# Kernel tuning notes

Measured on AMD Instinct MI355X. Metric: run time of the kernel, lower is better.

Reference implementation:

```python
import jax, jax.numpy as jnp
import numpy as np

D_MODEL = 1024
SEQ_LEN = 4096


def setup_inputs() -> dict:
    key = jax.random.key(0)
    ks = jax.random.split(key, 7)
    s = 1.0 / np.sqrt(D_MODEL)
    return {
        "x": jax.random.normal(ks[0], (SEQ_LEN, D_MODEL), dtype=jnp.float32),
        "w_q": jax.random.normal(ks[1], (D_MODEL, D_MODEL), dtype=jnp.float32) * s,
        "b_q": jax.random.normal(ks[2], (D_MODEL,), dtype=jnp.float32) * s,
        "w_k": jax.random.normal(ks[3], (D_MODEL, D_MODEL), dtype=jnp.float32) * s,
        "b_k": jax.random.normal(ks[4], (D_MODEL,), dtype=jnp.float32) * s,
        "w_v": jax.random.normal(ks[5], (D_MODEL, D_MODEL), dtype=jnp.float32) * s,
        "b_v": jax.random.normal(ks[6], (D_MODEL,), dtype=jnp.float32) * s,
    }


def reference(x, w_q, b_q, w_k, b_k, w_v, b_v):
    # q/k/v: [S, D]; torch Linear computes x @ W.T + b, weights here stored as [D, D]
    q = x @ w_q.T + b_q
    k = x @ w_k.T + b_k
    v = x @ w_v.T + b_v
    temperature = jnp.asarray(D_MODEL, dtype=x.dtype) ** 0.5
    # scores: [S, S]
    attn = jax.nn.softmax((q / temperature) @ k.T, axis=-1)
    # dropout is identity in eval mode
    return attn @ v
```

## Files before the change

kernel.cpp:

```cpp
#include <hip/hip_runtime.h>
#include <hip/hip_bf16.h>
#include <stdint.h>

#define SEQ 4096
#define DM  1024

typedef __attribute__((ext_vector_type(8))) short  s16x8;
typedef __attribute__((ext_vector_type(8))) _Float16 h16x8;
typedef __attribute__((ext_vector_type(4))) float  f32x4;

__device__ __forceinline__ ushort f2bf(float f) {
    union { float f; uint32_t u; } x; x.f = f;
    uint32_t r = x.u + 0x7fffu + ((x.u >> 16) & 1u);
    return (ushort)(r >> 16);
}

__device__ __forceinline__ void gload16(const void* g, void* l) {
    __builtin_amdgcn_global_load_lds(
        (const __attribute__((address_space(1))) void*)g,
        (__attribute__((address_space(3))) void*)l,
        16, 0, 0);
}

__global__ __launch_bounds__(256) void cvt_bf16(const float* __restrict__ in,
                                                ushort* __restrict__ out, int n4) {
    int i = blockIdx.x * blockDim.x + threadIdx.x;
    if (i < n4) {
        float4 v = ((const float4*)in)[i];
        ushort4 o;
        o.x = f2bf(v.x); o.y = f2bf(v.y); o.z = f2bf(v.z); o.w = f2bf(v.w);
        ((ushort4*)out)[i] = o;
    }
}

__global__ __launch_bounds__(512, 1)
void gemm256_score(const ushort* __restrict__ Q, const ushort* __restrict__ Km,
                   _Float16* __restrict__ S)
{
    constexpr int NT = DM / 64;
    constexpr int TOTAL_H = NT * 4;
    __shared__ ushort lds_u[65536];
    char* lb = (char*)lds_u;

    const int wg = blockIdx.x;
    const int logical = (wg & 7) * 32 + (wg >> 3);
    const int bx = logical & 15;
    const int by = logical >> 4;
    const int m0 = by * 256, n0 = bx * 256;

    const int tid = threadIdx.x;
    const int w = tid >> 6, l = tid & 63;
    const int wr = w >> 2, wc = w & 3;
    const int lm = l & 15;
    const int khb = (l >> 4) * 16;

    const ushort* Ab = Q  + (size_t)m0 * DM;
    const ushort* Bb = Km + (size_t)n0 * DM;

    const int in0 = tid * 16, in1 = 8192 + tid * 16;
    const int b0 = in0 ^ (((in0 >> 9) & 1) << 5);
    const int b1 = in1 ^ (((in1 >> 9) & 1) << 5);
    const int r0_ = b0 >> 6, c0_ = (b0 & 63) >> 1;
    const int r1_ = b1 >> 6, c1_ = (b1 & 63) >> 1;

    const int swzb = ((lm >> 3) & 1) << 5;
    const int aoff = (((wr * 128 + lm) * 64 + khb) ^ swzb);
    const int boff = (((wc * 64 + lm) * 64 + khb) ^ swzb);

    f32x4 acc[8][4] = {};
    s16x8 bq[4];

#define RBASE(buf, region) ((buf) * 65536 + (region) * 16384)

#define STAGE_H(g) do { \
    const int hidx_ = (g) - 1; const int tile_ = hidx_ >> 2; const int reg_ = hidx_ & 3; \
    const ushort* mp_ = (reg_ & 1) ? Bb : Ab; \
    const int colb_ = tile_ * 64 + (reg_ >> 1) * 32; \
    char* dst_ = lb + RBASE(tile_ & 1, reg_); \
    gload16(mp_ + (size_t)r0_ * DM + colb_ + c0_, dst_ + in0); \
    gload16(mp_ + (size_t)r1_ * DM + colb_ + c1_, dst_ + in1); \
} while (0)

#define PHASE(ph, kt2) do { \
    constexpr int kk_   = (((ph) - 1) >> 1) & 1; \
    constexpr int mh_   = ((ph) - 1) & 1; \
    constexpr int rbuf_ = ((ph) <= 4) ? 0 : 1; \
    constexpr int areg_ = kk_ * 2; \
    constexpr int breg_ = kk_ * 2 + 1; \
    s16x8 aq[4]; \
    if (mh_ == 0) { \
        _Pragma("unroll") \
        for (int nj = 0; nj < 4; ++nj) \
            bq[nj] = *(const s16x8*)(lb + RBASE(rbuf_, breg_) + boff + nj * 1024); \
    } \
    _Pragma("unroll") \
    for (int i = 0; i < 4; ++i) \
        aq[i] = *(const s16x8*)(lb + RBASE(rbuf_, areg_) + aoff + (mh_ * 4 + i) * 1024); \
    { const int g_ = (kt2) * 8 + (ph) + 6; if (g_ <= TOTAL_H) STAGE_H(g_); } \
    __builtin_amdgcn_s_barrier(); \
    asm volatile("s_waitcnt lgkmcnt(0)" ::: "memory"); \
    __builtin_amdgcn_sched_barrier(0); \
    __builtin_amdgcn_s_setprio(1); \
    _Pragma("unroll") \
    for (int i = 0; i < 4; ++i) { \
        _Pragma("unroll") \
        for (int nj = 0; nj < 4; ++nj) \
            acc[mh_ * 4 + i][nj] = __builtin_amdgcn_mfma_f32_16x16x32_bf16( \
                aq[i], bq[nj], acc[mh_ * 4 + i][nj], 0, 0, 0); \
    } \
    __builtin_amdgcn_s_setprio(0); \
    if ((ph) == 4 || (ph) == 8) asm volatile("s_waitcnt vmcnt(4)" ::: "memory"); \
    __builtin_amdgcn_s_barrier(); \
} while (0)

    STAGE_H(1); STAGE_H(2); STAGE_H(3); STAGE_H(4); STAGE_H(5); STAGE_H(6);
    asm volatile("s_waitcnt vmcnt(4)" ::: "memory");
    __builtin_amdgcn_s_barrier();

    for (int kt2 = 0; kt2 < NT / 2; ++kt2) {
        PHASE(1, kt2); PHASE(2, kt2); PHASE(3, kt2); PHASE(4, kt2);
        PHASE(5, kt2); PHASE(6, kt2); PHASE(7, kt2); PHASE(8, kt2);
    }

    const int er0 = m0 + wr * 128 + (l >> 4) * 4;
    const int ec0 = n0 + wc * 64 + lm;
#pragma unroll
    for (int mi = 0; mi < 8; ++mi)
#pragma unroll
        for (int nj = 0; nj < 4; ++nj)
#pragma unroll
            for (int r = 0; r < 4; ++r)
                S[(size_t)(er0 + mi * 16 + r) * SEQ + ec0 + nj * 16] =
                    (_Float16)acc[mi][nj][r];
#undef PHASE
#undef STAGE_H
#undef RBASE
}

template<int BIAS_MODE, int OUT_MODE>
__global__ __launch_bounds__(256)
void gemm128(const ushort* __restrict__ A, int lda,
             const ushort* __restrict__ B, int ldb,
             const float* __restrict__ bias,
             void* __restrict__ Cout, int ldc,
             int K, float scale, int nbx)
{
    __shared__ ushort lds_u[32768];
    char* lb = (char*)lds_u;

    const int nwg = gridDim.x;
    const int wg  = blockIdx.x;
    const int logical = (wg & 7) * (nwg >> 3) + (wg >> 3);
    const int bx = logical % nbx, by = logical / nbx;
    const int m0 = by * 128, n0 = bx * 128;

    const int tid = threadIdx.x;
    const int w = tid >> 6, l = tid & 63;
    const int wm = (w >> 1) * 64, wn = (w & 1) * 64;
    const int lm = l & 15;
    const int khb = (l >> 4) * 16;
    const int swzb = ((lm >> 3) & 1) << 5;
    const int aoff = ((wm + lm) * 64 + khb) ^ swzb;
    const int boff = ((wn + lm) * 64 + khb) ^ swzb;

    int rr[4], cc[4];
#pragma unroll
    for (int i = 0; i < 4; ++i) {
        const int rest = (i & 1) * 4096 + tid * 16;
        const int b = rest ^ (((rest >> 9) & 1) << 5);
        rr[i] = b >> 6; cc[i] = (b & 63) >> 1;
    }

#define STAGE128(t_, buf_) do { \
    const int colt_ = (t_) * 64; \
    _Pragma("unroll") \
    for (int i = 0; i < 4; ++i) { \
        const int ldso_ = (i >> 1) * 8192 + (i & 1) * 4096 + tid * 16; \
        gload16(A + (size_t)(m0 + rr[i]) * lda + colt_ + (i >> 1) * 32 + cc[i], \
                lb + (buf_) * 32768 + ldso_); \
        gload16(B + (size_t)(n0 + rr[i]) * ldb + colt_ + (i >> 1) * 32 + cc[i], \
                lb + (buf_) * 32768 + 16384 + ldso_); \
    } \
} while (0)

    f32x4 acc[4][4] = {};

#define COMPUTE128(buf_) do { \
    _Pragma("unroll") \
    for (int kk = 0; kk < 2; ++kk) { \
        s16x8 a_[4], b_[4]; \
        _Pragma("unroll") \
        for (int i = 0; i < 4; ++i) \
            a_[i] = *(const s16x8*)(lb + (buf_) * 32768 + kk * 8192 + aoff + i * 1024); \
        _Pragma("unroll") \
        for (int j = 0; j < 4; ++j) \
            b_[j] = *(const s16x8*)(lb + (buf_) * 32768 + 16384 + kk * 8192 + boff + j * 1024); \
        _Pragma("unroll") \
        for (int i = 0; i < 4; ++i) { \
            _Pragma("unroll") \
            for (int j = 0; j < 4; ++j) \
                acc[i][j] = __builtin_amdgcn_mfma_f32_16x16x32_bf16(a_[i], b_[j], acc[i][j], 0, 0, 0); \
        } \
    } \
} while (0)

    const int NT = K / 64;
    STAGE128(0, 0);
    __syncthreads();
    int t = 0;
    for (; t + 2 < NT; t += 2) {
        STAGE128(t + 1, 1); COMPUTE128(0); __syncthreads();
        STAGE128(t + 2, 0); COMPUTE128(1); __syncthreads();
    }
    STAGE128(NT - 1, 1); COMPUTE128(0); __syncthreads();
    COMPUTE128(1);

    const int r0 = m0 + wm + ((l >> 4) << 2);
    const int c0 = n0 + wn + lm;
#pragma unroll
    for (int i = 0; i < 4; ++i) {
#pragma unroll
        for (int j = 0; j < 4; ++j) {
#pragma unroll
            for (int r = 0; r < 4; ++r) {
                const int row = r0 + i * 16 + r;
                const int col = c0 + j * 16;
                float v = acc[i][j][r];
                if (BIAS_MODE == 1) v += bias[col];
                if (BIAS_MODE == 2) v += bias[row];
                v *= scale;
                if (OUT_MODE == 0) ((float*)Cout)[(size_t)row * ldc + col] = v;
                else               ((ushort*)Cout)[(size_t)row * ldc + col] = f2bf(v);
            }
        }
    }
#undef STAGE128
#undef COMPUTE128
}

__global__ __launch_bounds__(256) void softmax_rows(void* __restrict__ Sbase) {
    const int row = blockIdx.x;
    const int tid = threadIdx.x;
    const _Float16* srow = (const _Float16*)Sbase + (size_t)row * SEQ;

    float f[16];
#pragma unroll
    for (int j = 0; j < 2; ++j) {
        h16x8 v = *(const h16x8*)(srow + (size_t)(tid + j * 256) * 8);
#pragma unroll
        for (int e = 0; e < 8; ++e) f[j * 8 + e] = (float)v[e];
    }

    float m = f[0];
#pragma unroll
    for (int i = 1; i < 16; ++i) m = fmaxf(m, f[i]);
#pragma unroll
    for (int off = 32; off > 0; off >>= 1) m = fmaxf(m, __shfl_xor(m, off));

    __shared__ float redm[4], reds[4];
    const int w = tid >> 6, l = tid & 63;
    if (l == 0) redm[w] = m;
    __syncthreads();
    m = fmaxf(fmaxf(redm[0], redm[1]), fmaxf(redm[2], redm[3]));

    float s = 0.f;
#pragma unroll
    for (int i = 0; i < 16; ++i) { f[i] = __expf(f[i] - m); s += f[i]; }
#pragma unroll
    for (int off = 32; off > 0; off >>= 1) s += __shfl_xor(s, off);
    if (l == 0) reds[w] = s;
    __syncthreads();
    s = (reds[0] + reds[1]) + (reds[2] + reds[3]);
    const float inv = 1.0f / s;

    ushort* prow = (ushort*)Sbase + (size_t)row * SEQ;
#pragma unroll
    for (int j = 0; j < 2; ++j) {
        s16x8 o;
#pragma unroll
        for (int e = 0; e < 8; ++e) o[e] = (short)f2bf(f[j * 8 + e] * inv);
        *(s16x8*)(prow + (size_t)(tid + j * 256) * 8) = o;
    }
}

extern "C" void kernel_launch(void* const* d_in, const int* in_sizes, int n_in,
                              void* d_out, int out_size, void* d_ws, size_t ws_size,
                              hipStream_t stream)
{
    const float* x  = (const float*)d_in[0];
    const float* wq = (const float*)d_in[1];
    const float* bq = (const float*)d_in[2];
    const float* wk = (const float*)d_in[3];
    const float* bk = (const float*)d_in[4];
    const float* wv = (const float*)d_in[5];
    const float* bv = (const float*)d_in[6];

    char* ws = (char*)d_ws;
    const size_t MB = 1024 * 1024;
    ushort* Qb  = (ushort*)(ws);
    ushort* Kb  = (ushort*)(ws + 8 * MB);
    ushort* Vt  = (ushort*)(ws + 16 * MB);
    void*   Sm  = (void*)(ws + 24 * MB);
    ushort* P   = (ushort*)(ws + 24 * MB);
    ushort* xb  = (ushort*)(ws + 24 * MB);
    ushort* wqb = (ushort*)(ws + 32 * MB);
    ushort* wkb = (ushort*)(ws + 34 * MB);
    ushort* wvb = (ushort*)(ws + 36 * MB);

    cvt_bf16<<<dim3((SEQ * DM / 4 + 255) / 256), dim3(256), 0, stream>>>(x, xb, SEQ * DM / 4);
    cvt_bf16<<<dim3((DM * DM / 4 + 255) / 256), dim3(256), 0, stream>>>(wq, wqb, DM * DM / 4);
    cvt_bf16<<<dim3((DM * DM / 4 + 255) / 256), dim3(256), 0, stream>>>(wk, wkb, DM * DM / 4);
    cvt_bf16<<<dim3((DM * DM / 4 + 255) / 256), dim3(256), 0, stream>>>(wv, wvb, DM * DM / 4);

    const dim3 blk(256);
    gemm128<1, 1><<<dim3(256), blk, 0, stream>>>(xb, DM, wqb, DM, bq, Qb, DM, DM, 0.03125f, 8);
    gemm128<1, 1><<<dim3(256), blk, 0, stream>>>(xb, DM, wkb, DM, bk, Kb, DM, DM, 1.0f, 8);
    gemm128<2, 1><<<dim3(256), blk, 0, stream>>>(wvb, DM, xb, DM, bv, Vt, SEQ, DM, 1.0f, 32);

    gemm256_score<<<dim3(256), dim3(512), 0, stream>>>(Qb, Kb, (_Float16*)Sm);

    softmax_rows<<<dim3(SEQ), blk, 0, stream>>>(Sm);

    gemm128<0, 0><<<dim3(256), blk, 0, stream>>>(P, SEQ, Vt, SEQ, nullptr, d_out, DM, SEQ, 1.0f, 8);
}
```

Measured before the change: 161.6 us.

## Fuse conversions and Q/K projections, split-K the PV GEMM with a reduction

The four bf16 conversion launches become a single cvt_all kernel, and the Q and K projections become one 512-block launch. The 256-wide score GEMM is templated so it can also run the P·V product as a 256x128 tile, split-K in two halves, writing fp16 partials that a new reduce2 kernel sums into the fp32 output. This cuts launch count and gives the final GEMM a larger-tile pipelined kernel with better reuse. In exchange, partial sums are rounded to fp16, which loses precision, and the extra partial-buffer traffic must be read back by the reduction.

```diff
diff --git a/kernel.cpp b/kernel.cpp
--- a/kernel.cpp
+++ b/kernel.cpp
@@ -22,31 +22,62 @@
         16, 0, 0);
 }
 
-__global__ __launch_bounds__(256) void cvt_bf16(const float* __restrict__ in,
-                                                ushort* __restrict__ out, int n4) {
-    int i = blockIdx.x * blockDim.x + threadIdx.x;
-    if (i < n4) {
-        float4 v = ((const float4*)in)[i];
-        ushort4 o;
-        o.x = f2bf(v.x); o.y = f2bf(v.y); o.z = f2bf(v.z); o.w = f2bf(v.w);
-        ((ushort4*)out)[i] = o;
-    }
-}
-
+__global__ __launch_bounds__(256)
+void cvt_all(const float* __restrict__ x,  const float* __restrict__ wq,
+             const float* __restrict__ wk, const float* __restrict__ wv,
+             ushort* __restrict__ xb,  ushort* __restrict__ wqb,
+             ushort* __restrict__ wkb, ushort* __restrict__ wvb)
+{
+    int i = blockIdx.x * 256 + threadIdx.x;
+    const float* src; ushort* dst; int k;
+    if (i < 1048576) { src = x; dst = xb; k = i; }
+    else {
+        int j = i - 1048576; int w = j >> 18; k = j & 262143;
+        src = (w == 0) ? wq : (w == 1) ? wk : wv;
+        dst = (w == 0) ? wqb : (w == 1) ? wkb : wvb;
+    }
+    float4 v = ((const float4*)src)[k];
+    ushort4 o;
+    o.x = f2bf(v.x); o.y = f2bf(v.y); o.z = f2bf(v.z); o.w = f2bf(v.w);
+    ((ushort4*)dst)[k] = o;
+}
+
+template<int MODE>
 __global__ __launch_bounds__(512, 1)
-void gemm256_score(const ushort* __restrict__ Q, const ushort* __restrict__ Km,
-                   _Float16* __restrict__ S)
-{
-    constexpr int NT = DM / 64;
-    constexpr int TOTAL_H = NT * 4;
-    __shared__ ushort lds_u[65536];
+void gemm256p(const ushort* __restrict__ A, const ushort* __restrict__ B,
+              _Float16* __restrict__ Cbase, int lda, int ldc)
+{
+    constexpr int BN      = MODE ? 128 : 256;
+    constexpr int WN      = BN / 4;
+    constexpr int NJ      = BN / 64;
+    constexpr int REG_A   = 16384;
+    constexpr int REG_B   = BN * 32 * 2;
+    constexpr int BUFSZ   = 2 * (REG_A + REG_B);
+    constexpr int NTILES  = MODE ? 32 : 16;
+    constexpr int TOTAL_H = NTILES * 4;
+
+    __shared__ ushort lds_u[BUFSZ];
     char* lb = (char*)lds_u;
 
     const int wg = blockIdx.x;
     const int logical = (wg & 7) * 32 + (wg >> 3);
-    const int bx = logical & 15;
-    const int by = logical >> 4;
-    const int m0 = by * 256, n0 = bx * 256;
+    int m0, n0;
+    const ushort *Ab, *Bb;
+    _Float16* C;
+    if constexpr (MODE == 0) {
+        const int bx = logical & 15, by = logical >> 4;
+        m0 = by * 256; n0 = bx * 256;
+        Ab = A + (size_t)m0 * lda;
+        Bb = B + (size_t)n0 * lda;
+        C  = Cbase;
+    } else {
+        const int t = logical >> 1, ks = logical & 1;
+        const int by = t >> 3, bx = t & 7;
+        m0 = by * 256; n0 = bx * 128;
+        Ab = A + (size_t)m0 * lda + ks * 2048;
+        Bb = B + (size_t)n0 * lda + ks * 2048;
+        C  = Cbase + (size_t)ks * (4096 * 1024);
+    }
 
     const int tid = threadIdx.x;
     const int w = tid >> 6, l = tid & 63;
@@ -54,9 +85,6 @@
     const int lm = l & 15;
     const int khb = (l >> 4) * 16;
 
-    const ushort* Ab = Q  + (size_t)m0 * DM;
-    const ushort* Bb = Km + (size_t)n0 * DM;
-
     const int in0 = tid * 16, in1 = 8192 + tid * 16;
     const int b0 = in0 ^ (((in0 >> 9) & 1) << 5);
     const int b1 = in1 ^ (((in1 >> 9) & 1) << 5);
@@ -65,37 +93,49 @@
 
     const int swzb = ((lm >> 3) & 1) << 5;
     const int aoff = (((wr * 128 + lm) * 64 + khb) ^ swzb);
-    const int boff = (((wc * 64 + lm) * 64 + khb) ^ swzb);
-
-    f32x4 acc[8][4] = {};
-    s16x8 bq[4];
-
-#define RBASE(buf, region) ((buf) * 65536 + (region) * 16384)
+    const int boff = (((wc * WN + lm) * 64 + khb) ^ swzb);
+
+    f32x4 acc[8][NJ] = {};
+    s16x8 bq[NJ];
+
+    constexpr int roff0 = 0, roff1 = REG_A, roff2 = REG_A + REG_B,
+                  roff3 = 2 * REG_A + REG_B;
+
+#define ROFF(reg_) ((reg_) == 0 ? roff0 : (reg_) == 1 ? roff1 : (reg_) == 2 ? roff2 : roff3)
 
 #define STAGE_H(g) do { \
     const int hidx_ = (g) - 1; const int tile_ = hidx_ >> 2; const int reg_ = hidx_ & 3; \
-    const ushort* mp_ = (reg_ & 1) ? Bb : Ab; \
     const int colb_ = tile_ * 64 + (reg_ >> 1) * 32; \
-    char* dst_ = lb + RBASE(tile_ & 1, reg_); \
-    gload16(mp_ + (size_t)r0_ * DM + colb_ + c0_, dst_ + in0); \
-    gload16(mp_ + (size_t)r1_ * DM + colb_ + c1_, dst_ + in1); \
+    char* dst_ = lb + (tile_ & 1) * BUFSZ + ROFF(reg_); \
+    if (reg_ & 1) {  \
+        gload16(Bb + (size_t)r0_ * lda + colb_ + c0_, dst_ + in0); \
+        if constexpr (MODE == 0) gload16(Bb + (size_t)r1_ * lda + colb_ + c1_, dst_ + in1); \
+    } else {         \
+        gload16(Ab + (size_t)r0_ * lda + colb_ + c0_, dst_ + in0); \
+        gload16(Ab + (size_t)r1_ * lda + colb_ + c1_, dst_ + in1); \
+    } \
+} while (0)
+
+#define WAITVMC() do { \
+    if constexpr (MODE == 0) asm volatile("s_waitcnt vmcnt(4)" ::: "memory"); \
+    else                     asm volatile("s_waitcnt vmcnt(3)" ::: "memory"); \
 } while (0)
 
 #define PHASE(ph, kt2) do { \
     constexpr int kk_   = (((ph) - 1) >> 1) & 1; \
     constexpr int mh_   = ((ph) - 1) & 1; \
     constexpr int rbuf_ = ((ph) <= 4) ? 0 : 1; \
-    constexpr int areg_ = kk_ * 2; \
-    constexpr int breg_ = kk_ * 2 + 1; \
+    constexpr int aro_  = (kk_ == 0) ? roff0 : roff2; \
+    constexpr int bro_  = (kk_ == 0) ? roff1 : roff3; \
     s16x8 aq[4]; \
     if (mh_ == 0) { \
         _Pragma("unroll") \
-        for (int nj = 0; nj < 4; ++nj) \
-            bq[nj] = *(const s16x8*)(lb + RBASE(rbuf_, breg_) + boff + nj * 1024); \
+        for (int nj = 0; nj < NJ; ++nj) \
+            bq[nj] = *(const s16x8*)(lb + rbuf_ * BUFSZ + bro_ + boff + nj * 1024); \
     } \
     _Pragma("unroll") \
     for (int i = 0; i < 4; ++i) \
-        aq[i] = *(const s16x8*)(lb + RBASE(rbuf_, areg_) + aoff + (mh_ * 4 + i) * 1024); \
+        aq[i] = *(const s16x8*)(lb + rbuf_ * BUFSZ + aro_ + aoff + (mh_ * 4 + i) * 1024); \
     { const int g_ = (kt2) * 8 + (ph) + 6; if (g_ <= TOTAL_H) STAGE_H(g_); } \
     __builtin_amdgcn_s_barrier(); \
     asm volatile("s_waitcnt lgkmcnt(0)" ::: "memory"); \
@@ -104,37 +144,38 @@
     _Pragma("unroll") \
     for (int i = 0; i < 4; ++i) { \
         _Pragma("unroll") \
-        for (int nj = 0; nj < 4; ++nj) \
+        for (int nj = 0; nj < NJ; ++nj) \
             acc[mh_ * 4 + i][nj] = __builtin_amdgcn_mfma_f32_16x16x32_bf16( \
                 aq[i], bq[nj], acc[mh_ * 4 + i][nj], 0, 0, 0); \
     } \
     __builtin_amdgcn_s_setprio(0); \
-    if ((ph) == 4 || (ph) == 8) asm volatile("s_waitcnt vmcnt(4)" ::: "memory"); \
+    if ((ph) == 4 || (ph) == 8) WAITVMC(); \
     __builtin_amdgcn_s_barrier(); \
 } while (0)
 
     STAGE_H(1); STAGE_H(2); STAGE_H(3); STAGE_H(4); STAGE_H(5); STAGE_H(6);
-    asm volatile("s_waitcnt vmcnt(4)" ::: "memory");
+    WAITVMC();
     __builtin_amdgcn_s_barrier();
 
-    for (int kt2 = 0; kt2 < NT / 2; ++kt2) {
+    for (int kt2 = 0; kt2 < NTILES / 2; ++kt2) {
         PHASE(1, kt2); PHASE(2, kt2); PHASE(3, kt2); PHASE(4, kt2);
         PHASE(5, kt2); PHASE(6, kt2); PHASE(7, kt2); PHASE(8, kt2);
     }
 
     const int er0 = m0 + wr * 128 + (l >> 4) * 4;
-    const int ec0 = n0 + wc * 64 + lm;
+    const int ec0 = n0 + wc * WN + lm;
 #pragma unroll
     for (int mi = 0; mi < 8; ++mi)
 #pragma unroll
-        for (int nj = 0; nj < 4; ++nj)
+        for (int nj = 0; nj < NJ; ++nj)
 #pragma unroll
             for (int r = 0; r < 4; ++r)
-                S[(size_t)(er0 + mi * 16 + r) * SEQ + ec0 + nj * 16] =
+                C[(size_t)(er0 + mi * 16 + r) * ldc + ec0 + nj * 16] =
                     (_Float16)acc[mi][nj][r];
 #undef PHASE
 #undef STAGE_H
-#undef RBASE
+#undef WAITVMC
+#undef ROFF
 }
 
 template<int BIAS_MODE, int OUT_MODE>
@@ -238,6 +279,106 @@
 #undef COMPUTE128
 }
 
+__global__ __launch_bounds__(256)
+void gemm128_qk(const ushort* __restrict__ Aq,
+                const ushort* __restrict__ Wq, const ushort* __restrict__ Wk,
+                const float* __restrict__ bqv, const float* __restrict__ bkv,
+                ushort* __restrict__ Qo, ushort* __restrict__ Ko)
+{
+    __shared__ ushort lds_u[32768];
+    char* lb = (char*)lds_u;
+
+    const int logical = (blockIdx.x & 7) * 64 + (blockIdx.x >> 3);
+    const int bxg = logical & 15, by = logical >> 4;
+    const bool isQ = bxg < 8;
+    const int bx = isQ ? bxg : bxg - 8;
+    const ushort* B = isQ ? Wq : Wk;
+    const float* bias = isQ ? bqv : bkv;
+    ushort* Cout = isQ ? Qo : Ko;
+    const float scale = isQ ? 0.03125f : 1.0f;
+    const int m0 = by * 128, n0 = bx * 128;
+    const ushort* A = Aq;
+
+    const int tid = threadIdx.x;
+    const int w = tid >> 6, l = tid & 63;
+    const int wm = (w >> 1) * 64, wn = (w & 1) * 64;
+    const int lm = l & 15;
+    const int khb = (l >> 4) * 16;
+    const int swzb = ((lm >> 3) & 1) << 5;
+    const int aoff = ((wm + lm) * 64 + khb) ^ swzb;
+    const int boff = ((wn + lm) * 64 + khb) ^ swzb;
+
+    int rr[4], cc[4];
+#pragma unroll
+    for (int i = 0; i < 4; ++i) {
+        const int rest = (i & 1) * 4096 + tid * 16;
+        const int b = rest ^ (((rest >> 9) & 1) << 5);
+        rr[i] = b >> 6; cc[i] = (b & 63) >> 1;
+    }
+
+#define STAGEQK(t_, buf_) do { \
+    const int colt_ = (t_) * 64; \
+    _Pragma("unroll") \
+    for (int i = 0; i < 4; ++i) { \
+        const int ldso_ = (i >> 1) * 8192 + (i & 1) * 4096 + tid * 16; \
+        gload16(A + (size_t)(m0 + rr[i]) * DM + colt_ + (i >> 1) * 32 + cc[i], \
+                lb + (buf_) * 32768 + ldso_); \
+        gload16(B + (size_t)(n0 + rr[i]) * DM + colt_ + (i >> 1) * 32 + cc[i], \
+                lb + (buf_) * 32768 + 16384 + ldso_); \
+    } \
+} while (0)
+
+    f32x4 acc[4][4] = {};
+
+#define COMPUTEQK(buf_) do { \
+    _Pragma("unroll") \
+    for (int kk = 0; kk < 2; ++kk) { \
+        s16x8 a_[4], b_[4]; \
+        _Pragma("unroll") \
+        for (int i = 0; i < 4; ++i) \
+            a_[i] = *(const s16x8*)(lb + (buf_) * 32768 + kk * 8192 + aoff + i * 1024); \
+        _Pragma("unroll") \
+        for (int j = 0; j < 4; ++j) \
+            b_[j] = *(const s16x8*)(lb + (buf_) * 32768 + 16384 + kk * 8192 + boff + j * 1024); \
+        _Pragma("unroll") \
+        for (int i = 0; i < 4; ++i) { \
+            _Pragma("unroll") \
+            for (int j = 0; j < 4; ++j) \
+                acc[i][j] = __builtin_amdgcn_mfma_f32_16x16x32_bf16(a_[i], b_[j], acc[i][j], 0, 0, 0); \
+        } \
+    } \
+} while (0)
+
+    const int NT = DM / 64;
+    STAGEQK(0, 0);
+    __syncthreads();
+    int t = 0;
+    for (; t + 2 < NT; t += 2) {
+        STAGEQK(t + 1, 1); COMPUTEQK(0); __syncthreads();
+        STAGEQK(t + 2, 0); COMPUTEQK(1); __syncthreads();
+    }
+    STAGEQK(NT - 1, 1); COMPUTEQK(0); __syncthreads();
+    COMPUTEQK(1);
+
+    const int r0 = m0 + wm + ((l >> 4) << 2);
+    const int c0 = n0 + wn + lm;
+#pragma unroll
+    for (int i = 0; i < 4; ++i) {
+#pragma unroll
+        for (int j = 0; j < 4; ++j) {
+#pragma unroll
+            for (int r = 0; r < 4; ++r) {
+                const int row = r0 + i * 16 + r;
+                const int col = c0 + j * 16;
+                float v = (acc[i][j][r] + bias[col]) * scale;
+                Cout[(size_t)row * DM + col] = f2bf(v);
+            }
+        }
+    }
+#undef STAGEQK
+#undef COMPUTEQK
+}
+
 __global__ __launch_bounds__(256) void softmax_rows(void* __restrict__ Sbase) {
     const int row = blockIdx.x;
     const int tid = threadIdx.x;
@@ -281,6 +422,22 @@
         for (int e = 0; e < 8; ++e) o[e] = (short)f2bf(f[j * 8 + e] * inv);
         *(s16x8*)(prow + (size_t)(tid + j * 256) * 8) = o;
     }
+}
+
+__global__ __launch_bounds__(256)
+void reduce2(const _Float16* __restrict__ p0, const _Float16* __restrict__ p1,
+             float* __restrict__ out)
+{
+    const size_t i = (size_t)(blockIdx.x * 256 + threadIdx.x) * 8;
+    h16x8 a = *(const h16x8*)(p0 + i);
+    h16x8 b = *(const h16x8*)(p1 + i);
+    float4 o0, o1;
+    o0.x = (float)a[0] + (float)b[0]; o0.y = (float)a[1] + (float)b[1];
+    o0.z = (float)a[2] + (float)b[2]; o0.w = (float)a[3] + (float)b[3];
+    o1.x = (float)a[4] + (float)b[4]; o1.y = (float)a[5] + (float)b[5];
+    o1.z = (float)a[6] + (float)b[6]; o1.w = (float)a[7] + (float)b[7];
+    *(float4*)(out + i) = o0;
+    *(float4*)(out + i + 4) = o1;
 }
 
 extern "C" void kernel_launch(void* const* d_in, const int* in_sizes, int n_in,
@@ -297,29 +454,30 @@
 
     char* ws = (char*)d_ws;
     const size_t MB = 1024 * 1024;
-    ushort* Qb  = (ushort*)(ws);
-    ushort* Kb  = (ushort*)(ws + 8 * MB);
-    ushort* Vt  = (ushort*)(ws + 16 * MB);
-    void*   Sm  = (void*)(ws + 24 * MB);
-    ushort* P   = (ushort*)(ws + 24 * MB);
-    ushort* xb  = (ushort*)(ws + 24 * MB);
-    ushort* wqb = (ushort*)(ws + 32 * MB);
-    ushort* wkb = (ushort*)(ws + 34 * MB);
-    ushort* wvb = (ushort*)(ws + 36 * MB);
-
-    cvt_bf16<<<dim3((SEQ * DM / 4 + 255) / 256), dim3(256), 0, stream>>>(x, xb, SEQ * DM / 4);
-    cvt_bf16<<<dim3((DM * DM / 4 + 255) / 256), dim3(256), 0, stream>>>(wq, wqb, DM * DM / 4);
-    cvt_bf16<<<dim3((DM * DM / 4 + 255) / 256), dim3(256), 0, stream>>>(wk, wkb, DM * DM / 4);
-    cvt_bf16<<<dim3((DM * DM / 4 + 255) / 256), dim3(256), 0, stream>>>(wv, wvb, DM * DM / 4);
-
-    const dim3 blk(256);
-    gemm128<1, 1><<<dim3(256), blk, 0, stream>>>(xb, DM, wqb, DM, bq, Qb, DM, DM, 0.03125f, 8);
-    gemm128<1, 1><<<dim3(256), blk, 0, stream>>>(xb, DM, wkb, DM, bk, Kb, DM, DM, 1.0f, 8);
-    gemm128<2, 1><<<dim3(256), blk, 0, stream>>>(wvb, DM, xb, DM, bv, Vt, SEQ, DM, 1.0f, 32);
-
-    gemm256_score<<<dim3(256), dim3(512), 0, stream>>>(Qb, Kb, (_Float16*)Sm);
-
-    softmax_rows<<<dim3(SEQ), blk, 0, stream>>>(Sm);
-
-    gemm128<0, 0><<<dim3(256), blk, 0, stream>>>(P, SEQ, Vt, SEQ, nullptr, d_out, DM, SEQ, 1.0f, 8);
-}
+    ushort*   Qb  = (ushort*)(ws);
+    ushort*   Kb  = (ushort*)(ws + 8 * MB);
+    ushort*   Vt  = (ushort*)(ws + 16 * MB);
+    void*     Sm  = (void*)(ws + 24 * MB);
+    ushort*   P   = (ushort*)(ws + 24 * MB);
+    ushort*   xb  = (ushort*)(ws + 24 * MB);
+    ushort*   wqb = (ushort*)(ws + 32 * MB);
+    ushort*   wkb = (ushort*)(ws + 34 * MB);
+    ushort*   wvb = (ushort*)(ws + 36 * MB);
+    _Float16* Pp  = (_Float16*)(ws);
+
+    cvt_all<<<dim3(7168), dim3(256), 0, stream>>>(x, wq, wk, wv, xb, wqb, wkb, wvb);
+
+    gemm128_qk<<<dim3(512), dim3(256), 0, stream>>>(xb, wqb, wkb, bq, bk, Qb, Kb);
+
+    gemm128<2, 1><<<dim3(256), dim3(256), 0, stream>>>(
+        wvb, DM, xb, DM, bv, Vt, SEQ, DM, 1.0f, 32);
+
+    gemm256p<0><<<dim3(256), dim3(512), 0, stream>>>(Qb, Kb, (_Float16*)Sm, DM, SEQ);
+
+    softmax_rows<<<dim3(SEQ), dim3(256), 0, stream>>>(Sm);
+
+    gemm256p<1><<<dim3(256), dim3(512), 0, stream>>>(P, Vt, Pp, SEQ, DM);
+
+    reduce2<<<dim3(2048), dim3(256), 0, stream>>>(Pp, Pp + (size_t)4096 * 1024,
+                                                  (float*)d_out);
+}
```

Result: faster. 142.0 us (-12.1%).
